# Optimization experiments

Hardware: AMD Instinct MI355X
Metric: run time of the kernel (lower is better)

Reference implementation:

```python
import jax, jax.numpy as jnp
import numpy as np

OBS_LEN, K, B, H, MID, NC, CIN = 12, 20, 2048, 128, 256, 2, 3

def setup_inputs() -> dict:
    key = jax.random.key(0)
    ks = jax.random.split(key, 12)
    w = lambda k, s: 0.1 * jax.random.normal(k, s, dtype=jnp.float32)
    return {
        'obs_traj_rel': jax.random.normal(ks[0], (OBS_LEN, B, CIN), dtype=jnp.float32),
        'pred_lstm_hidden': jax.random.normal(ks[1], (K, B, H), dtype=jnp.float32),
        'map_w0': w(ks[2], (H, MID)), 'map_b0': jnp.zeros((MID,), jnp.float32),
        'map_w1': w(ks[3], (MID, H)), 'map_b1': jnp.zeros((H,), jnp.float32),
        'w_ih': w(ks[4], (4 * H, NC)), 'w_hh': w(ks[5], (4 * H, H)),
        'b_ih': jnp.zeros((4 * H,), jnp.float32), 'b_hh': jnp.zeros((4 * H,), jnp.float32),
        'out_w': w(ks[6], (H, NC)), 'out_b': jnp.zeros((NC,), jnp.float32),
    }

def _hard_sigmoid(x):
    # torch F.hardsigmoid: clip(x/6 + 0.5, 0, 1)
    return jnp.clip(x / 6.0 + 0.5, 0.0, 1.0)

def reference(obs_traj_rel, pred_lstm_hidden, map_w0, map_b0, map_w1, map_b1,
              w_ih, w_hh, b_ih, b_hh, out_w, out_b):
    n_coord = out_w.shape[1]
    hdim = w_hh.shape[1]
    # mapping MLP on initial hidden state: [K, B, H]
    h = jax.nn.leaky_relu(pred_lstm_hidden @ map_w0 + map_b0, negative_slope=0.01)
    h = h @ map_w1 + map_b1
    c = jnp.zeros_like(h)
    # step i uses obs[i-1] (obs[0] at i=0), sliced to first n_coord channels
    inputs = jnp.concatenate([obs_traj_rel[:1], obs_traj_rel[:-1]], axis=0)[:, :, :n_coord]  # [T, B, nc]
    bias = b_ih + b_hh

    def step(carry, x_t):
        h, c = carry  # each [K, B, H]
        # x_t [B, nc] broadcast over samples K (same gates contribution for all K)
        gx = x_t @ w_ih.T  # [B, 4H]
        gates = gx[None, :, :] + h @ w_hh.T + bias  # [K, B, 4H]
        i, f, g, o = jnp.split(gates, 4, axis=-1)
        i = _hard_sigmoid(i); f = _hard_sigmoid(f)
        g = jnp.clip(g, -1.0, 1.0); o = _hard_sigmoid(o)
        c_new = f * c + i * g
        h_new = o * jnp.clip(c_new, -1.0, 1.0)
        out = h_new @ out_w + out_b  # [K, B, nc]
        return (h_new, c_new), out

    _, outs = jax.lax.scan(step, (h, c), inputs)
    return outs  # [obs_len, K, B, n_coord]
```

## Files before the change

kernel.cpp:

```cpp
#include <hip/hip_runtime.h>
#include <stdint.h>

#define OBS_LEN 12
#define KS 20
#define BB 2048
#define HD 128
#define MIDD 256
#define NCQ 2

#define WSW_OFF  0
#define WSM0_OFF 65536
#define WSM1_OFF 98304
#define WSO_OFF  131072
#define WS_ELEMS 133120

using f32x4  = __attribute__((ext_vector_type(4))) float;
using bf16x8 = __attribute__((ext_vector_type(8))) short;

static __device__ __forceinline__ short f2bf(float f){
  return __builtin_bit_cast(short, (__bf16)f);
}
static __device__ __forceinline__ uint32_t pack2(float a, float b){
  return (uint32_t)(uint16_t)f2bf(a) | ((uint32_t)(uint16_t)f2bf(b) << 16);
}
static __device__ __forceinline__ float hsig(float x){
  return fminf(fmaxf(fmaf(x, 0.16666666666666666f, 0.5f), 0.f), 1.f);
}
static __device__ __forceinline__ float clip1(float x){
  return fminf(fmaxf(x, -1.f), 1.f);
}
static __device__ __forceinline__ f32x4 mm(bf16x8 a, bf16x8 b, f32x4 c){
  return __builtin_amdgcn_mfma_f32_16x16x32_bf16(a, b, c, 0, 0, 0);
}
static __device__ __forceinline__ bf16x8 ldh(const uint16_t* buf, int row, int q, int p){
  return *reinterpret_cast<const bf16x8*>(&buf[(row*HD + q*32 + p*8) ^ ((row&7)*8)]);
}
static __device__ __forceinline__ bf16x8 lda(const uint16_t* buf, int row, int q, int p){
  return *reinterpret_cast<const bf16x8*>(&buf[(row*MIDD + q*32 + p*8) ^ ((row&7)*8)]);
}

__global__ void CRMF_prep_kernel(const float* __restrict__ mw0,
                                 const float* __restrict__ mw1,
                                 const float* __restrict__ whh,
                                 const float* __restrict__ oww,
                                 uint16_t* __restrict__ ws)
{
  int f = blockIdx.x*256 + threadIdx.x;
  if (f >= 16640) return;
  bf16x8 out;
  int dst;
  if (f < 8192){
    int l=f&63, q=(f>>6)&3, gate=(f>>8)&3, w=f>>10;
    int col = gate*128 + w*16 + (l&15);
    const float* s = whh + col*HD + q*32 + ((l>>4)&3)*8;
    #pragma unroll
    for (int j=0;j<8;++j) out[j] = f2bf(s[j]);
    dst = WSW_OFF + f*8;
  } else if (f < 12288){
    int ff=f-8192; int l=ff&63, q=(ff>>6)&3, ct=(ff>>8)&1, w=ff>>9;
    int col = w*32 + ct*16 + (l&15);
    int r0 = q*32 + ((l>>4)&3)*8;
    #pragma unroll
    for (int j=0;j<8;++j) out[j] = f2bf(mw0[(r0+j)*MIDD + col]);
    dst = WSM0_OFF + ff*8;
  } else if (f < 16384){
    int ff=f-12288; int l=ff&63, q=(ff>>6)&7, w=ff>>9;
    int col = w*16 + (l&15);
    int r0 = q*32 + ((l>>4)&3)*8;
    #pragma unroll
    for (int j=0;j<8;++j) out[j] = f2bf(mw1[(r0+j)*HD + col]);
    dst = WSM1_OFF + ff*8;
  } else {
    int ff=f-16384; int l=ff&63, q=ff>>6;
    int lnn=l&15; int r0 = q*32 + ((l>>4)&3)*8;
    #pragma unroll
    for (int j=0;j<8;++j) out[j] = (lnn<NCQ) ? f2bf(oww[(r0+j)*NCQ + lnn]) : (short)0;
    dst = WSO_OFF + ff*8;
  }
  *reinterpret_cast<bf16x8*>(&ws[dst]) = out;
}

template<bool FWS>
__global__ __launch_bounds__(512, 2)
void CRMF_35296041239144_kernel(
    const float* __restrict__ obs,  const float* __restrict__ pred,
    const float* __restrict__ mw0,  const float* __restrict__ mb0,
    const float* __restrict__ mw1,  const float* __restrict__ mb1,
    const float* __restrict__ wih,  const float* __restrict__ whh,
    const float* __restrict__ bih,  const float* __restrict__ bhh,
    const float* __restrict__ oww,  const float* __restrict__ obb,
    const uint16_t* __restrict__ ws,
    float* __restrict__ outp)
{
  __shared__ __align__(16) uint16_t hbuf[2][32*HD];
  __shared__ __align__(16) uint16_t abuf[32*MIDD];
  __shared__ __align__(16) uint16_t ofrag[4*64*8];
  __shared__ float2 xbuf[OBS_LEN][32];
  __shared__ float  ostage[OBS_LEN][64];

  const int tid = threadIdx.x;
  const int w   = tid >> 6;
  const int l   = tid & 63;
  const int p   = (tid >> 4) & 3;
  const int ln  = tid & 15;
  const int wofs = w * 16;
  const bool w7 = (w == 7);

  const int b     = blockIdx.x;
  const int b0    = (b & 63) * 32;
  const int kslot = b >> 6;

  if (tid < OBS_LEN*32){
    int t = tid >> 5, cc = tid & 31;
    int st = t ? (t-1) : 0;
    const float* pp = obs + ((size_t)st*BB + b0 + cc)*3;
    xbuf[t][cc] = make_float2(pp[0], pp[1]);
  }
  if (tid < 256){
    bf16x8 wf;
    if constexpr (FWS){
      wf = *reinterpret_cast<const bf16x8*>(&ws[WSO_OFF + tid*8]);
    } else {
      int q = tid >> 6, ll = tid & 63;
      int lln = ll & 15, pp2 = (ll >> 4) & 3;
      #pragma unroll
      for (int j=0; j<8; ++j)
        wf[j] = (lln < NCQ) ? f2bf(oww[(q*32+pp2*8+j)*NCQ + lln]) : (short)0;
    }
    *reinterpret_cast<bf16x8*>(&ofrag[tid*8]) = wf;
  }
  const float obv = (ln < NCQ) ? obb[ln] : 0.f;

  bf16x8 wfrag[4][4];
  #pragma unroll
  for (int gate=0; gate<4; ++gate){
    #pragma unroll
    for (int q=0; q<4; ++q){
      if constexpr (FWS){
        wfrag[gate][q] = *reinterpret_cast<const bf16x8*>(
            &ws[WSW_OFF + (((w*4+gate)*4+q)*64 + l)*8]);
      } else {
        int col = gate*128 + wofs + ln;
        const float* s = whh + col*HD + q*32 + p*8;
        float4 f0 = *reinterpret_cast<const float4*>(s);
        float4 f1 = *reinterpret_cast<const float4*>(s+4);
        bf16x8 wf;
        wf[0]=f2bf(f0.x); wf[1]=f2bf(f0.y); wf[2]=f2bf(f0.z); wf[3]=f2bf(f0.w);
        wf[4]=f2bf(f1.x); wf[5]=f2bf(f1.y); wf[6]=f2bf(f1.z); wf[7]=f2bf(f1.w);
        wfrag[gate][q] = wf;
      }
    }
  }
  float wihA[4], wihB[4], biasv[4];
  #pragma unroll
  for (int gate=0; gate<4; ++gate){
    int col = gate*128 + wofs + ln;
    wihA[gate]  = wih[col*2];
    wihB[gate]  = wih[col*2+1];
    biasv[gate] = bih[col] + bhh[col];
  }

  #pragma unroll 1
  for (int c=0; c<5; ++c){
    const int kk = kslot*5 + c;

    __syncthreads();
    {
      const float* src = pred + ((size_t)(kk*BB + b0))*HD;
      #pragma unroll
      for (int it=0; it<2; ++it){
        int u = tid + it*512;
        int row = u >> 5, c4 = (u & 31)*4;
        float4 v = *reinterpret_cast<const float4*>(src + row*HD + c4);
        int e = (row*HD + c4) ^ ((row&7)*8);
        *reinterpret_cast<uint32_t*>(&hbuf[0][e])   = pack2(v.x, v.y);
        *reinterpret_cast<uint32_t*>(&hbuf[0][e+2]) = pack2(v.z, v.w);
      }
    }
    __syncthreads();

    {
      f32x4 acc1[2][2];
      #pragma unroll
      for (int ct=0; ct<2; ++ct){
        float mb = mb0[w*32 + ct*16 + ln];
        f32x4 v = {mb,mb,mb,mb};
        acc1[0][ct]=v; acc1[1][ct]=v;
      }
      #pragma unroll
      for (int q=0; q<4; ++q){
        bf16x8 af0 = ldh(hbuf[0], ln, q, p), af1 = ldh(hbuf[0], 16+ln, q, p);
        #pragma unroll
        for (int ct=0; ct<2; ++ct){
          bf16x8 wf;
          if constexpr (FWS){
            wf = *reinterpret_cast<const bf16x8*>(
                &ws[WSM0_OFF + (((w*2+ct)*4+q)*64 + l)*8]);
          } else {
            #pragma unroll
            for (int j=0; j<8; ++j)
              wf[j] = f2bf(mw0[(q*32+p*8+j)*MIDD + (w*32 + ct*16 + ln)]);
          }
          acc1[0][ct] = mm(af0, wf, acc1[0][ct]);
          acc1[1][ct] = mm(af1, wf, acc1[1][ct]);
        }
      }
      #pragma unroll
      for (int rt=0; rt<2; ++rt)
      #pragma unroll
      for (int ct=0; ct<2; ++ct)
      #pragma unroll
      for (int r=0; r<4; ++r){
        float v = acc1[rt][ct][r];
        v = (v>0.f)? v : 0.01f*v;
        int row = rt*16 + p*4 + r;
        abuf[(row*MIDD + w*32 + ct*16 + ln) ^ ((row&7)*8)] = (uint16_t)f2bf(v);
      }
    }
    __syncthreads();

    float c_[2][4];
    {
      f32x4 acc2[2];
      float mb = mb1[wofs + ln];
      f32x4 v = {mb,mb,mb,mb};
      acc2[0]=v; acc2[1]=v;
      #pragma unroll
      for (int q=0; q<8; ++q){
        bf16x8 af0 = lda(abuf, ln, q, p), af1 = lda(abuf, 16+ln, q, p);
        bf16x8 wf;
        if constexpr (FWS){
          wf = *reinterpret_cast<const bf16x8*>(&ws[WSM1_OFF + ((w*8+q)*64 + l)*8]);
        } else {
          #pragma unroll
          for (int j=0; j<8; ++j)
            wf[j] = f2bf(mw1[(q*32+p*8+j)*HD + wofs + ln]);
        }
        acc2[0] = mm(af0, wf, acc2[0]);
        acc2[1] = mm(af1, wf, acc2[1]);
      }
      #pragma unroll
      for (int rt=0; rt<2; ++rt)
      #pragma unroll
      for (int r=0; r<4; ++r){
        int row = rt*16 + p*4 + r;
        hbuf[0][(row*HD + wofs + ln) ^ ((row&7)*8)] = (uint16_t)f2bf(acc2[rt][r]);
        c_[rt][r] = 0.f;
      }
    }
    __syncthreads();

    #pragma unroll 1
    for (int t=0; t<OBS_LEN; ++t){
      const int cur = t & 1, nxt = cur ^ 1;
      f32x4 acc[2][4];
      #pragma unroll
      for (int rt=0; rt<2; ++rt){
        #pragma unroll
        for (int r=0; r<4; ++r){
          float2 xv = xbuf[t][rt*16 + p*4 + r];
          #pragma unroll
          for (int gate=0; gate<4; ++gate)
            acc[rt][gate][r] = fmaf(xv.x, wihA[gate], fmaf(xv.y, wihB[gate], biasv[gate]));
        }
      }
      f32x4 a8[2];
      if (w7 && t>0){ f32x4 v={obv,obv,obv,obv}; a8[0]=v; a8[1]=v; }
      #pragma unroll
      for (int q=0; q<4; ++q){
        bf16x8 af0 = ldh(hbuf[cur], ln, q, p), af1 = ldh(hbuf[cur], 16+ln, q, p);
        #pragma unroll
        for (int gate=0; gate<4; ++gate){
          acc[0][gate] = mm(af0, wfrag[gate][q], acc[0][gate]);
          acc[1][gate] = mm(af1, wfrag[gate][q], acc[1][gate]);
        }
        if (w7 && t>0){
          bf16x8 of = *reinterpret_cast<const bf16x8*>(&ofrag[(q*64 + l)*8]);
          a8[0] = mm(af0, of, a8[0]);
          a8[1] = mm(af1, of, a8[1]);
        }
      }
      if (w7 && t>0 && ln<NCQ){
        #pragma unroll
        for (int rt=0; rt<2; ++rt)
        #pragma unroll
        for (int r=0; r<4; ++r)
          ostage[t-1][(rt*16 + p*4 + r)*NCQ + ln] = a8[rt][r];
      }
      #pragma unroll
      for (int rt=0; rt<2; ++rt)
      #pragma unroll
      for (int r=0; r<4; ++r){
        float iv = hsig(acc[rt][0][r]);
        float fv = hsig(acc[rt][1][r]);
        float gv = clip1(acc[rt][2][r]);
        float ov = hsig(acc[rt][3][r]);
        float cv = fmaf(fv, c_[rt][r], iv*gv);
        c_[rt][r] = cv;
        int row = rt*16 + p*4 + r;
        hbuf[nxt][(row*HD + wofs + ln) ^ ((row&7)*8)] = (uint16_t)f2bf(ov * clip1(cv));
      }
      __syncthreads();
    }

    if (w7){
      f32x4 o0 = {obv,obv,obv,obv}, o1 = o0;
      #pragma unroll
      for (int q=0; q<4; ++q){
        bf16x8 af0 = ldh(hbuf[0], ln, q, p), af1 = ldh(hbuf[0], 16+ln, q, p);
        bf16x8 of = *reinterpret_cast<const bf16x8*>(&ofrag[(q*64 + l)*8]);
        o0 = mm(af0, of, o0);
        o1 = mm(af1, of, o1);
      }
      if (ln < NCQ){
        #pragma unroll
        for (int r=0; r<4; ++r){
          ostage[11][(     p*4 + r)*NCQ + ln] = o0[r];
          ostage[11][(16 + p*4 + r)*NCQ + ln] = o1[r];
        }
      }
    }
    __syncthreads();

    for (int u = tid; u < OBS_LEN*64; u += 512){
      int t = u >> 6, e = u & 63;
      outp[((size_t)(t*KS + kk)*BB + b0)*NCQ + e] = ostage[t][e];
    }
  }
}

extern "C" void kernel_launch(void* const* d_in, const int* in_sizes, int n_in,
                              void* d_out, int out_size, void* d_ws, size_t ws_size,
                              hipStream_t stream) {
  (void)in_sizes; (void)n_in; (void)out_size;
  const float* obs  = (const float*)d_in[0];
  const float* pred = (const float*)d_in[1];
  const float* mw0  = (const float*)d_in[2];
  const float* mb0  = (const float*)d_in[3];
  const float* mw1  = (const float*)d_in[4];
  const float* mb1  = (const float*)d_in[5];
  const float* wih  = (const float*)d_in[6];
  const float* whh  = (const float*)d_in[7];
  const float* bih  = (const float*)d_in[8];
  const float* bhh  = (const float*)d_in[9];
  const float* oww  = (const float*)d_in[10];
  const float* obb  = (const float*)d_in[11];
  float* outp = (float*)d_out;

  if (ws_size >= (size_t)WS_ELEMS * sizeof(uint16_t)){
    uint16_t* ws = (uint16_t*)d_ws;
    CRMF_prep_kernel<<<dim3(65), dim3(256), 0, stream>>>(mw0, mw1, whh, oww, ws);
    CRMF_35296041239144_kernel<true><<<dim3(256), dim3(512), 0, stream>>>(
        obs, pred, mw0, mb0, mw1, mb1, wih, whh, bih, bhh, oww, obb,
        (const uint16_t*)ws, outp);
  } else {
    CRMF_35296041239144_kernel<false><<<dim3(256), dim3(512), 0, stream>>>(
        obs, pred, mw0, mb0, mw1, mb1, wih, whh, bih, bhh, oww, obb,
        (const uint16_t*)nullptr, outp);
  }
}
```

Measured before the change: 176.9 us.

## Split K-chunks across twice as many blocks and reload recurrent weights from global

The fast path launches 512 blocks instead of 256. Each pair of blocks splits the five K samples 3/2, so more CUs are busy. Instead of keeping the recurrent weight fragments in registers, they are reloaded from the preprocessed workspace at every timestep. An opaque asm offset stops the compiler from hoisting those loads back into registers, which cuts register use so launch bounds can rise to 4 blocks per CU. In exchange, each step now does repeated L1/L2 weight loads, and the work is unbalanced between the 3-chunk and 2-chunk blocks.

```diff
diff --git a/kernel.cpp b/kernel.cpp
--- a/kernel.cpp
+++ b/kernel.cpp
@@ -80,15 +80,12 @@
   *reinterpret_cast<bf16x8*>(&ws[dst]) = out;
 }
 
-template<bool FWS>
-__global__ __launch_bounds__(512, 2)
-void CRMF_35296041239144_kernel(
+__global__ __launch_bounds__(512, 4)
+void CRMF_fast_kernel(
     const float* __restrict__ obs,  const float* __restrict__ pred,
-    const float* __restrict__ mw0,  const float* __restrict__ mb0,
-    const float* __restrict__ mw1,  const float* __restrict__ mb1,
-    const float* __restrict__ wih,  const float* __restrict__ whh,
-    const float* __restrict__ bih,  const float* __restrict__ bhh,
-    const float* __restrict__ oww,  const float* __restrict__ obb,
+    const float* __restrict__ mb0,  const float* __restrict__ mb1,
+    const float* __restrict__ wih,  const float* __restrict__ bih,
+    const float* __restrict__ bhh,  const float* __restrict__ obb,
     const uint16_t* __restrict__ ws,
     float* __restrict__ outp)
 {
@@ -104,11 +101,15 @@
   const int p   = (tid >> 4) & 3;
   const int ln  = tid & 15;
   const int wofs = w * 16;
-  const bool w7 = (w == 7);
-
-  const int b     = blockIdx.x;
-  const int b0    = (b & 63) * 32;
-  const int kslot = b >> 6;
+
+  const int b    = blockIdx.x;
+  const int pr   = b >> 1;
+  const int odd  = b & 1;
+  const int b0   = (pr & 63) * 32;
+  const int kslot= pr >> 6;
+  const int nch  = odd ? 2 : 3;
+  const int cbase= odd ? 3 : 0;
+  const bool wOut = (w == (odd ? 4 : 7));
 
   if (tid < OBS_LEN*32){
     int t = tid >> 5, cc = tid & 31;
@@ -116,41 +117,11 @@
     const float* pp = obs + ((size_t)st*BB + b0 + cc)*3;
     xbuf[t][cc] = make_float2(pp[0], pp[1]);
   }
-  if (tid < 256){
-    bf16x8 wf;
-    if constexpr (FWS){
-      wf = *reinterpret_cast<const bf16x8*>(&ws[WSO_OFF + tid*8]);
-    } else {
-      int q = tid >> 6, ll = tid & 63;
-      int lln = ll & 15, pp2 = (ll >> 4) & 3;
-      #pragma unroll
-      for (int j=0; j<8; ++j)
-        wf[j] = (lln < NCQ) ? f2bf(oww[(q*32+pp2*8+j)*NCQ + lln]) : (short)0;
-    }
-    *reinterpret_cast<bf16x8*>(&ofrag[tid*8]) = wf;
-  }
+  if (tid < 256)
+    *reinterpret_cast<bf16x8*>(&ofrag[tid*8]) =
+        *reinterpret_cast<const bf16x8*>(&ws[WSO_OFF + tid*8]);
   const float obv = (ln < NCQ) ? obb[ln] : 0.f;
 
-  bf16x8 wfrag[4][4];
-  #pragma unroll
-  for (int gate=0; gate<4; ++gate){
-    #pragma unroll
-    for (int q=0; q<4; ++q){
-      if constexpr (FWS){
-        wfrag[gate][q] = *reinterpret_cast<const bf16x8*>(
-            &ws[WSW_OFF + (((w*4+gate)*4+q)*64 + l)*8]);
-      } else {
-        int col = gate*128 + wofs + ln;
-        const float* s = whh + col*HD + q*32 + p*8;
-        float4 f0 = *reinterpret_cast<const float4*>(s);
-        float4 f1 = *reinterpret_cast<const float4*>(s+4);
-        bf16x8 wf;
-        wf[0]=f2bf(f0.x); wf[1]=f2bf(f0.y); wf[2]=f2bf(f0.z); wf[3]=f2bf(f0.w);
-        wf[4]=f2bf(f1.x); wf[5]=f2bf(f1.y); wf[6]=f2bf(f1.z); wf[7]=f2bf(f1.w);
-        wfrag[gate][q] = wf;
-      }
-    }
-  }
   float wihA[4], wihB[4], biasv[4];
   #pragma unroll
   for (int gate=0; gate<4; ++gate){
@@ -161,8 +132,10 @@
   }
 
   #pragma unroll 1
-  for (int c=0; c<5; ++c){
-    const int kk = kslot*5 + c;
+  for (int i=0; i<nch; ++i){
+    const int kk = kslot*5 + cbase + i;
+    int coff = 0;
+    asm volatile("" : "+s"(coff));
 
     __syncthreads();
     {
@@ -192,15 +165,8 @@
         bf16x8 af0 = ldh(hbuf[0], ln, q, p), af1 = ldh(hbuf[0], 16+ln, q, p);
         #pragma unroll
         for (int ct=0; ct<2; ++ct){
-          bf16x8 wf;
-          if constexpr (FWS){
-            wf = *reinterpret_cast<const bf16x8*>(
-                &ws[WSM0_OFF + (((w*2+ct)*4+q)*64 + l)*8]);
-          } else {
-            #pragma unroll
-            for (int j=0; j<8; ++j)
-              wf[j] = f2bf(mw0[(q*32+p*8+j)*MIDD + (w*32 + ct*16 + ln)]);
-          }
+          bf16x8 wf = *reinterpret_cast<const bf16x8*>(
+              &ws[WSM0_OFF + (((w*2+ct)*4+q)*64 + l)*8 + coff]);
           acc1[0][ct] = mm(af0, wf, acc1[0][ct]);
           acc1[1][ct] = mm(af1, wf, acc1[1][ct]);
         }
@@ -228,14 +194,8 @@
       #pragma unroll
       for (int q=0; q<8; ++q){
         bf16x8 af0 = lda(abuf, ln, q, p), af1 = lda(abuf, 16+ln, q, p);
-        bf16x8 wf;
-        if constexpr (FWS){
-          wf = *reinterpret_cast<const bf16x8*>(&ws[WSM1_OFF + ((w*8+q)*64 + l)*8]);
-        } else {
-          #pragma unroll
-          for (int j=0; j<8; ++j)
-            wf[j] = f2bf(mw1[(q*32+p*8+j)*HD + wofs + ln]);
-        }
+        bf16x8 wf = *reinterpret_cast<const bf16x8*>(
+            &ws[WSM1_OFF + ((w*8+q)*64 + l)*8 + coff]);
         acc2[0] = mm(af0, wf, acc2[0]);
         acc2[1] = mm(af1, wf, acc2[1]);
       }
@@ -252,6 +212,8 @@
 
     #pragma unroll 1
     for (int t=0; t<OBS_LEN; ++t){
+      int toff = 0;
+      asm volatile("" : "+s"(toff));
       const int cur = t & 1, nxt = cur ^ 1;
       f32x4 acc[2][4];
       #pragma unroll
@@ -265,22 +227,24 @@
         }
       }
       f32x4 a8[2];
-      if (w7 && t>0){ f32x4 v={obv,obv,obv,obv}; a8[0]=v; a8[1]=v; }
+      if (wOut && t>0){ f32x4 v={obv,obv,obv,obv}; a8[0]=v; a8[1]=v; }
       #pragma unroll
       for (int q=0; q<4; ++q){
         bf16x8 af0 = ldh(hbuf[cur], ln, q, p), af1 = ldh(hbuf[cur], 16+ln, q, p);
         #pragma unroll
         for (int gate=0; gate<4; ++gate){
-          acc[0][gate] = mm(af0, wfrag[gate][q], acc[0][gate]);
-          acc[1][gate] = mm(af1, wfrag[gate][q], acc[1][gate]);
-        }
-        if (w7 && t>0){
+          bf16x8 wf = *reinterpret_cast<const bf16x8*>(
+              &ws[WSW_OFF + (((w*4+gate)*4+q)*64 + l)*8 + toff]);
+          acc[0][gate] = mm(af0, wf, acc[0][gate]);
+          acc[1][gate] = mm(af1, wf, acc[1][gate]);
+        }
+        if (wOut && t>0){
           bf16x8 of = *reinterpret_cast<const bf16x8*>(&ofrag[(q*64 + l)*8]);
           a8[0] = mm(af0, of, a8[0]);
           a8[1] = mm(af1, of, a8[1]);
         }
       }
-      if (w7 && t>0 && ln<NCQ){
+      if (wOut && t>0 && ln<NCQ){
         #pragma unroll
         for (int rt=0; rt<2; ++rt)
         #pragma unroll
@@ -303,7 +267,7 @@
       __syncthreads();
     }
 
-    if (w7){
+    if (wOut){
       f32x4 o0 = {obv,obv,obv,obv}, o1 = o0;
       #pragma unroll
       for (int q=0; q<4; ++q){
@@ -322,6 +286,225 @@
     }
     __syncthreads();
 
+    for (int u = tid; u < OBS_LEN*64; u += 512){
+      int t = u >> 6, e = u & 63;
+      outp[((size_t)(t*KS + kk)*BB + b0)*NCQ + e] = ostage[t][e];
+    }
+  }
+}
+
+__global__ __launch_bounds__(512, 2)
+void CRMF_safe_kernel(
+    const float* __restrict__ obs,  const float* __restrict__ pred,
+    const float* __restrict__ mw0,  const float* __restrict__ mb0,
+    const float* __restrict__ mw1,  const float* __restrict__ mb1,
+    const float* __restrict__ wih,  const float* __restrict__ whh,
+    const float* __restrict__ bih,  const float* __restrict__ bhh,
+    const float* __restrict__ oww,  const float* __restrict__ obb,
+    float* __restrict__ outp)
+{
+  __shared__ __align__(16) uint16_t hbuf[2][32*HD];
+  __shared__ __align__(16) uint16_t abuf[32*MIDD];
+  __shared__ __align__(16) uint16_t ofrag[4*64*8];
+  __shared__ float2 xbuf[OBS_LEN][32];
+  __shared__ float  ostage[OBS_LEN][64];
+
+  const int tid = threadIdx.x;
+  const int w   = tid >> 6;
+  const int l   = tid & 63;
+  const int p   = (tid >> 4) & 3;
+  const int ln  = tid & 15;
+  const int wofs = w * 16;
+  const bool w7 = (w == 7);
+
+  const int b     = blockIdx.x;
+  const int b0    = (b & 63) * 32;
+  const int kslot = b >> 6;
+
+  if (tid < OBS_LEN*32){
+    int t = tid >> 5, cc = tid & 31;
+    int st = t ? (t-1) : 0;
+    const float* pp = obs + ((size_t)st*BB + b0 + cc)*3;
+    xbuf[t][cc] = make_float2(pp[0], pp[1]);
+  }
+  if (tid < 256){
+    int q = tid >> 6, ll = tid & 63;
+    int lln = ll & 15, pp2 = (ll >> 4) & 3;
+    bf16x8 wf;
+    #pragma unroll
+    for (int j=0; j<8; ++j)
+      wf[j] = (lln < NCQ) ? f2bf(oww[(q*32+pp2*8+j)*NCQ + lln]) : (short)0;
+    *reinterpret_cast<bf16x8*>(&ofrag[tid*8]) = wf;
+  }
+  const float obv = (ln < NCQ) ? obb[ln] : 0.f;
+
+  bf16x8 wfrag[4][4];
+  float wihA[4], wihB[4], biasv[4];
+  #pragma unroll
+  for (int gate=0; gate<4; ++gate){
+    int col = gate*128 + wofs + ln;
+    wihA[gate]  = wih[col*2];
+    wihB[gate]  = wih[col*2+1];
+    biasv[gate] = bih[col] + bhh[col];
+    #pragma unroll
+    for (int q=0; q<4; ++q){
+      const float* s = whh + col*HD + q*32 + p*8;
+      float4 f0 = *reinterpret_cast<const float4*>(s);
+      float4 f1 = *reinterpret_cast<const float4*>(s+4);
+      bf16x8 wf;
+      wf[0]=f2bf(f0.x); wf[1]=f2bf(f0.y); wf[2]=f2bf(f0.z); wf[3]=f2bf(f0.w);
+      wf[4]=f2bf(f1.x); wf[5]=f2bf(f1.y); wf[6]=f2bf(f1.z); wf[7]=f2bf(f1.w);
+      wfrag[gate][q] = wf;
+    }
+  }
+
+  #pragma unroll 1
+  for (int c=0; c<5; ++c){
+    const int kk = kslot*5 + c;
+    __syncthreads();
+    {
+      const float* src = pred + ((size_t)(kk*BB + b0))*HD;
+      #pragma unroll
+      for (int it=0; it<2; ++it){
+        int u = tid + it*512;
+        int row = u >> 5, c4 = (u & 31)*4;
+        float4 v = *reinterpret_cast<const float4*>(src + row*HD + c4);
+        int e = (row*HD + c4) ^ ((row&7)*8);
+        *reinterpret_cast<uint32_t*>(&hbuf[0][e])   = pack2(v.x, v.y);
+        *reinterpret_cast<uint32_t*>(&hbuf[0][e+2]) = pack2(v.z, v.w);
+      }
+    }
+    __syncthreads();
+    {
+      f32x4 acc1[2][2];
+      #pragma unroll
+      for (int ct=0; ct<2; ++ct){
+        float mb = mb0[w*32 + ct*16 + ln];
+        f32x4 v = {mb,mb,mb,mb};
+        acc1[0][ct]=v; acc1[1][ct]=v;
+      }
+      #pragma unroll
+      for (int q=0; q<4; ++q){
+        bf16x8 af0 = ldh(hbuf[0], ln, q, p), af1 = ldh(hbuf[0], 16+ln, q, p);
+        #pragma unroll
+        for (int ct=0; ct<2; ++ct){
+          bf16x8 wf;
+          #pragma unroll
+          for (int j=0; j<8; ++j)
+            wf[j] = f2bf(mw0[(q*32+p*8+j)*MIDD + (w*32 + ct*16 + ln)]);
+          acc1[0][ct] = mm(af0, wf, acc1[0][ct]);
+          acc1[1][ct] = mm(af1, wf, acc1[1][ct]);
+        }
+      }
+      #pragma unroll
+      for (int rt=0; rt<2; ++rt)
+      #pragma unroll
+      for (int ct=0; ct<2; ++ct)
+      #pragma unroll
+      for (int r=0; r<4; ++r){
+        float v = acc1[rt][ct][r];
+        v = (v>0.f)? v : 0.01f*v;
+        int row = rt*16 + p*4 + r;
+        abuf[(row*MIDD + w*32 + ct*16 + ln) ^ ((row&7)*8)] = (uint16_t)f2bf(v);
+      }
+    }
+    __syncthreads();
+    float c_[2][4];
+    {
+      f32x4 acc2[2];
+      float mb = mb1[wofs + ln];
+      f32x4 v = {mb,mb,mb,mb};
+      acc2[0]=v; acc2[1]=v;
+      #pragma unroll
+      for (int q=0; q<8; ++q){
+        bf16x8 af0 = lda(abuf, ln, q, p), af1 = lda(abuf, 16+ln, q, p);
+        bf16x8 wf;
+        #pragma unroll
+        for (int j=0; j<8; ++j)
+          wf[j] = f2bf(mw1[(q*32+p*8+j)*HD + wofs + ln]);
+        acc2[0] = mm(af0, wf, acc2[0]);
+        acc2[1] = mm(af1, wf, acc2[1]);
+      }
+      #pragma unroll
+      for (int rt=0; rt<2; ++rt)
+      #pragma unroll
+      for (int r=0; r<4; ++r){
+        int row = rt*16 + p*4 + r;
+        hbuf[0][(row*HD + wofs + ln) ^ ((row&7)*8)] = (uint16_t)f2bf(acc2[rt][r]);
+        c_[rt][r] = 0.f;
+      }
+    }
+    __syncthreads();
+    #pragma unroll 1
+    for (int t=0; t<OBS_LEN; ++t){
+      const int cur = t & 1, nxt = cur ^ 1;
+      f32x4 acc[2][4];
+      #pragma unroll
+      for (int rt=0; rt<2; ++rt){
+        #pragma unroll
+        for (int r=0; r<4; ++r){
+          float2 xv = xbuf[t][rt*16 + p*4 + r];
+          #pragma unroll
+          for (int gate=0; gate<4; ++gate)
+            acc[rt][gate][r] = fmaf(xv.x, wihA[gate], fmaf(xv.y, wihB[gate], biasv[gate]));
+        }
+      }
+      f32x4 a8[2];
+      if (w7 && t>0){ f32x4 v={obv,obv,obv,obv}; a8[0]=v; a8[1]=v; }
+      #pragma unroll
+      for (int q=0; q<4; ++q){
+        bf16x8 af0 = ldh(hbuf[cur], ln, q, p), af1 = ldh(hbuf[cur], 16+ln, q, p);
+        #pragma unroll
+        for (int gate=0; gate<4; ++gate){
+          acc[0][gate] = mm(af0, wfrag[gate][q], acc[0][gate]);
+          acc[1][gate] = mm(af1, wfrag[gate][q], acc[1][gate]);
+        }
+        if (w7 && t>0){
+          bf16x8 of = *reinterpret_cast<const bf16x8*>(&ofrag[(q*64 + l)*8]);
+          a8[0] = mm(af0, of, a8[0]);
+          a8[1] = mm(af1, of, a8[1]);
+        }
+      }
+      if (w7 && t>0 && ln<NCQ){
+        #pragma unroll
+        for (int rt=0; rt<2; ++rt)
+        #pragma unroll
+        for (int r=0; r<4; ++r)
+          ostage[t-1][(rt*16 + p*4 + r)*NCQ + ln] = a8[rt][r];
+      }
+      #pragma unroll
+      for (int rt=0; rt<2; ++rt)
+      #pragma unroll
+      for (int r=0; r<4; ++r){
+        float iv = hsig(acc[rt][0][r]);
+        float fv = hsig(acc[rt][1][r]);
+        float gv = clip1(acc[rt][2][r]);
+        float ov = hsig(acc[rt][3][r]);
+        float cv = fmaf(fv, c_[rt][r], iv*gv);
+        c_[rt][r] = cv;
+        int row = rt*16 + p*4 + r;
+        hbuf[nxt][(row*HD + wofs + ln) ^ ((row&7)*8)] = (uint16_t)f2bf(ov * clip1(cv));
+      }
+      __syncthreads();
+    }
+    if (w7){
+      f32x4 o0 = {obv,obv,obv,obv}, o1 = o0;
+      #pragma unroll
+      for (int q=0; q<4; ++q){
+        bf16x8 af0 = ldh(hbuf[0], ln, q, p), af1 = ldh(hbuf[0], 16+ln, q, p);
+        bf16x8 of = *reinterpret_cast<const bf16x8*>(&ofrag[(q*64 + l)*8]);
+        o0 = mm(af0, of, o0);
+        o1 = mm(af1, of, o1);
+      }
+      if (ln < NCQ){
+        #pragma unroll
+        for (int r=0; r<4; ++r){
+          ostage[11][(     p*4 + r)*NCQ + ln] = o0[r];
+          ostage[11][(16 + p*4 + r)*NCQ + ln] = o1[r];
+        }
+      }
+    }
+    __syncthreads();
     for (int u = tid; u < OBS_LEN*64; u += 512){
       int t = u >> 6, e = u & 63;
       outp[((size_t)(t*KS + kk)*BB + b0)*NCQ + e] = ostage[t][e];
@@ -350,12 +533,10 @@
   if (ws_size >= (size_t)WS_ELEMS * sizeof(uint16_t)){
     uint16_t* ws = (uint16_t*)d_ws;
     CRMF_prep_kernel<<<dim3(65), dim3(256), 0, stream>>>(mw0, mw1, whh, oww, ws);
-    CRMF_35296041239144_kernel<true><<<dim3(256), dim3(512), 0, stream>>>(
-        obs, pred, mw0, mb0, mw1, mb1, wih, whh, bih, bhh, oww, obb,
-        (const uint16_t*)ws, outp);
+    CRMF_fast_kernel<<<dim3(512), dim3(512), 0, stream>>>(
+        obs, pred, mb0, mb1, wih, bih, bhh, obb, (const uint16_t*)ws, outp);
   } else {
-    CRMF_35296041239144_kernel<false><<<dim3(256), dim3(512), 0, stream>>>(
-        obs, pred, mw0, mb0, mw1, mb1, wih, whh, bih, bhh, oww, obb,
-        (const uint16_t*)nullptr, outp);
-  }
-}
+    CRMF_safe_kernel<<<dim3(256), dim3(512), 0, stream>>>(
+        obs, pred, mw0, mb0, mw1, mb1, wih, whh, bih, bhh, oww, obb, outp);
+  }
+}
```

New measurement: 234.8 us. 32.7% more time.
